# Kernel tuning notes

Measured on AMD Instinct MI355X. Metric: run time of the kernel, lower is better.

## Reference

```python
import jax, jax.numpy as jnp
import numpy as np
from itertools import combinations

B, T, D = 2, 2048, 1024
H, PD = 16, 4
DH = D // H
PAIRS = list(combinations(range(PD), 2))  # 6 pairs -> plucker_dim 6

_J6 = jnp.array([[0, 0, 0, 0, 0, 1], [0, 0, 0, 0, -1, 0], [0, 0, 0, 1, 0, 0],
                 [0, 0, 1, 0, 0, 0], [0, -1, 0, 0, 0, 0], [1, 0, 0, 0, 0, 0]],
                dtype=jnp.float32)


def exterior(p1, p2):
    # p1, p2: [B,T,H,PD] -> normalized Plucker coords [B,T,H,6]
    parts = [p1[..., i] * p2[..., j] - p1[..., j] * p2[..., i] for i, j in PAIRS]
    L = jnp.stack(parts, axis=-1)
    n = jnp.maximum(jnp.linalg.norm(L, axis=-1, keepdims=True), 1e-12)
    return L / n


def setup_inputs() -> dict:
    key = jax.random.key(0)
    ks = jax.random.split(key, 16)
    s = 0.02
    inp = {
        'x': jax.random.normal(ks[0], (B, T, D), jnp.float32),
        'qkv_w': jax.random.normal(ks[1], (D, 3 * D), jnp.float32) * s,
        'qkv_b': jnp.zeros((3 * D,), jnp.float32),
        'w1_write': jax.random.normal(ks[2], (D, PD * H), jnp.float32) * s,
        'w2_write': jax.random.normal(ks[3], (D, PD * H), jnp.float32) * s,
        'w1_read': jax.random.normal(ks[4], (D, PD * H), jnp.float32) * s,
        'w2_read': jax.random.normal(ks[5], (D, PD * H), jnp.float32) * s,
        'memv_w': jax.random.normal(ks[6], (D, D), jnp.float32) * s,
        'memv_b': jnp.zeros((D,), jnp.float32),
        'memg_w': jax.random.normal(ks[7], (D, H), jnp.float32) * s,
        'memg_b': jnp.zeros((H,), jnp.float32),
        'mem_scale': jnp.full((H,), 0.1, jnp.float32),
        'out_w': jax.random.normal(ks[8], (D, D), jnp.float32) * s,
        'out_b': jnp.zeros((D,), jnp.float32),
        'J': _J6,
        'decays': jnp.array([0.95] * (H // 2) + [0.999] * (H - H // 2), jnp.float32),
    }
    return inp


def reference(x, qkv_w, qkv_b, w1_write, w2_write, w1_read, w2_read,
              memv_w, memv_b, memg_w, memg_b, mem_scale, out_w, out_b, J, decays):
    Bx, Tx, Dx = x.shape
    scale = DH ** -0.5

    # --- standard causal attention branch ---
    qkv = (x @ qkv_w + qkv_b).reshape(Bx, Tx, 3, H, DH)
    q, k, v = qkv[:, :, 0], qkv[:, :, 1], qkv[:, :, 2]  # [B,T,H,dh]
    scores = jnp.einsum('bihd,bjhd->bhij', q, k) * scale
    i = jnp.arange(Tx)
    causal = i[:, None] >= i[None, :]  # keep j <= i
    scores = jnp.where(causal[None, None], scores, -jnp.inf)
    attn = jax.nn.softmax(scores, axis=-1)
    seq_out = jnp.einsum('bhij,bjhd->bihd', attn, v).reshape(Bx, Tx, Dx)

    # --- Plucker memory branch ---
    x_prev = jnp.concatenate([jnp.zeros((Bx, 1, Dx), x.dtype), x[:, :-1]], axis=1)
    w1 = (x_prev @ w1_write).reshape(Bx, Tx, H, PD)
    w2 = (x @ w2_write).reshape(Bx, Tx, H, PD)
    write_lines = exterior(w1, w2)          # [B,T,H,6]
    r1 = (x @ w1_read).reshape(Bx, Tx, H, PD)
    r2 = (x @ w2_read).reshape(Bx, Tx, H, PD)
    read_lines = exterior(r1, r2)           # [B,T,H,6]

    Jw = jnp.einsum('bthi,ij->bthj', write_lines, J)
    incidence = jnp.einsum('bihp,bjhp->bhij', read_lines, Jw)  # [B,H,T,T]
    inc_sq = incidence ** 2

    diffs = i[:, None] - i[None, :]                      # [T,T]
    lower = diffs > 0                                    # strictly past (j < i)
    dsafe = jnp.where(lower, diffs, 0).astype(x.dtype)
    weights = jnp.where(lower[None], decays[:, None, None] ** dsafe[None], 0.0)  # [H,T,T]
    mem_score = jnp.sum(inc_sq * weights[None], axis=-1)  # [B,H,T]

    mem_val = x @ memv_w + memv_b                         # [B,T,D]
    gate = jax.nn.sigmoid(x @ memg_w + memg_b)            # [B,T,H]
    gated = jax.nn.sigmoid(mem_score.transpose(0, 2, 1) * mem_scale[None, None]) * gate
    gated = jnp.mean(gated, axis=-1, keepdims=True)       # [B,T,1]

    return (seq_out + gated * mem_val) @ out_w + out_b
```

## Files before the change

### kernel.cpp

```cpp
#include <hip/hip_runtime.h>

#define BT 4096
#define Dd 1024
#define Tt 2048

typedef __attribute__((ext_vector_type(8))) short bf16x8;
typedef __attribute__((ext_vector_type(4))) float f32x4;
typedef __attribute__((ext_vector_type(4))) unsigned u32x4;

__device__ __forceinline__ short f2bf(float f) {
  unsigned u = __builtin_bit_cast(unsigned, f);
  u = (u + 0x7FFFu + ((u >> 16) & 1u)) >> 16;
  return (short)u;
}
__device__ __forceinline__ float bf2f(short s) {
  unsigned u = ((unsigned)(unsigned short)s) << 16;
  return __builtin_bit_cast(float, u);
}
__device__ __forceinline__ unsigned cvt_pk_bf16(float a, float b) {
  unsigned r;
  asm("v_cvt_pk_bf16_f32 %0, %1, %2" : "=v"(r) : "v"(a), "v"(b));
  return r;
}

__device__ __forceinline__ void load_lds16(const void* gsrc, void* ldst) {
  __builtin_amdgcn_global_load_lds(
      (const __attribute__((address_space(1))) void*)gsrc,
      (__attribute__((address_space(3))) void*)ldst, 16, 0, 0);
}

__global__ __launch_bounds__(256) void k_wtall(
    const float* __restrict__ qkv_w, const float* __restrict__ memv_w,
    const float* __restrict__ out_w, const float* __restrict__ w1w,
    const float* __restrict__ w2w, const float* __restrict__ w1r,
    const float* __restrict__ w2r, const float* __restrict__ memg_w,
    short* __restrict__ WTall, short* __restrict__ WTout,
    const float* __restrict__ x, short* __restrict__ xb) {
  __shared__ float tile[64][65];
  const int bid = blockIdx.x;
  if (bid >= 1360) {
    int i = (bid - 1360) * 256 + threadIdx.x;
    float4 v = ((const float4*)x)[i];
    short4 o;
    o.x = f2bf(v.x); o.y = f2bf(v.y); o.z = f2bf(v.z); o.w = f2bf(v.w);
    ((short4*)xb)[i] = o;
    return;
  }
  const float* src;
  short* dst;
  int N, n0, k0, rowoff;
  if (bid < 768) {
    src = qkv_w; dst = WTall; N = 3072;
    n0 = (bid % 48) * 64; k0 = (bid / 48) * 64; rowoff = 0;
  } else if (bid < 1024) {
    int r = bid - 768;
    src = memv_w; dst = WTall; N = 1024;
    n0 = (r % 16) * 64; k0 = (r / 16) * 64; rowoff = 3072;
  } else if (bid < 1280) {
    int r = bid - 1024;
    src = out_w; dst = WTout; N = 1024;
    n0 = (r % 16) * 64; k0 = (r / 16) * 64; rowoff = 0;
  } else {
    int r = bid - 1280;
    int z = r / 16;
    src = z == 0 ? w1w : z == 1 ? w2w : z == 2 ? w1r : z == 3 ? w2r : memg_w;
    dst = WTall; N = (z == 4) ? 16 : 64;
    n0 = 0; k0 = (r % 16) * 64; rowoff = 4096 + z * 64;
  }
  const int c = threadIdx.x & 63, r4 = threadIdx.x >> 6;
#pragma unroll
  for (int i = 0; i < 16; ++i) {
    int r = i * 4 + r4;
    float v = 0.f;
    if (n0 + c < N) v = src[(size_t)(k0 + r) * N + n0 + c];
    tile[r][c] = v;
  }
  __syncthreads();
#pragma unroll
  for (int i = 0; i < 16; ++i) {
    int n = i * 4 + r4;
    if (n0 + n < N)
      dst[(size_t)(rowoff + n0 + n) * 1024 + k0 + c] = f2bf(tile[c][n]);
  }
}

__global__ __launch_bounds__(256, 4) void k_g128(
    const short* __restrict__ A, const short* __restrict__ Bt,
    const float* __restrict__ bias, const float* __restrict__ bias2,
    short* __restrict__ oq, short* __restrict__ ok_, short* __restrict__ ov,
    short* __restrict__ omv, float* __restrict__ ocs, int K) {
  __shared__ __align__(16) short lds[16384];
  const int tid = threadIdx.x;
  const int wid = tid >> 6, lane = tid & 63;
  const int wr = wid >> 1, wc = wid & 1;
  const int ql = lane & 15, g = lane >> 4;
  int wg = blockIdx.x, xcd = wg & 7, idx = wg >> 3;
  const int n_t = idx >> 2;
  const int m_t = xcd * 4 + (idx & 3);
  const int nkt = K >> 5;
  const int bm = m_t * 128, bn = n_t * 128;
  f32x4 acc[4][4] = {};

  const short* srcA[2];
  const short* srcB[2];
  short* dstA[2];
  short* dstB[2];
#pragma unroll
  for (int j = 0; j < 2; ++j) {
    int o16 = j * 256 + tid;
    int rr = o16 >> 2, u = o16 & 3;
    int sp = u ^ ((rr >> 1) & 3);
    srcA[j] = A + (size_t)(bm + rr) * K + sp * 8;
    srcB[j] = Bt + (size_t)(bn + rr) * K + sp * 8;
    dstA[j] = lds + o16 * 8;
    dstB[j] = lds + 8192 + o16 * 8;
  }
#define STG(D, KT)                                                            \
  do {                                                                        \
    const int k0s = (KT) << 5;                                                \
    _Pragma("unroll") for (int j = 0; j < 2; ++j) {                           \
      load_lds16(srcA[j] + k0s, dstA[j] + (D)*4096);                          \
      load_lds16(srcB[j] + k0s, dstB[j] + (D)*4096);                          \
    }                                                                         \
  } while (0)

  const int sw = (g ^ ((ql >> 1) & 3)) << 4;
  const char* bA = (const char*)lds + wr * 4096 + ql * 64 + sw;
  const char* bB = (const char*)lds + 16384 + wc * 4096 + ql * 64 + sw;

#define RD_A(DST, DOFF, MQ)                                                    \
  _Pragma("unroll") for (int mi = 0; mi < 2; ++mi)                             \
      DST[mi] = *(const bf16x8*)(bA + (DOFF) + (MQ)*2048 + mi * 1024);
#define RD_B(DST, DOFF, NQ)                                                    \
  _Pragma("unroll") for (int ni = 0; ni < 2; ++ni)                             \
      DST[ni] = *(const bf16x8*)(bB + (DOFF) + (NQ)*2048 + ni * 1024);
#define MFMA4(AF, BF, MQ, NQ)                                                  \
  _Pragma("unroll") for (int mi = 0; mi < 2; ++mi)                             \
      _Pragma("unroll") for (int ni = 0; ni < 2; ++ni)                         \
          acc[(MQ)*2 + mi][(NQ)*2 + ni] =                                      \
      __builtin_amdgcn_mfma_f32_16x16x32_bf16(                                 \
          BF[ni], AF[mi], acc[(MQ)*2 + mi][(NQ)*2 + ni], 0, 0, 0)

  STG(0, 0);

  for (int kt = 0; kt < nkt; ++kt) {
    const int d = kt & 1;
    const int dOff = d << 13;
    const bool s1 = kt + 1 < nkt;
    if (s1) {
      STG(d ^ 1, kt + 1);
      asm volatile("s_waitcnt vmcnt(4)" ::: "memory");
    } else {
      asm volatile("s_waitcnt vmcnt(0)" ::: "memory");
    }
    __builtin_amdgcn_sched_barrier(0);
    __builtin_amdgcn_s_barrier();
    bf16x8 a0[2], a1[2], b0[2], b1[2];
    RD_A(a0, dOff, 0);
    RD_A(a1, dOff, 1);
    RD_B(b0, dOff, 0);
    RD_B(b1, dOff, 1);
    asm volatile("s_waitcnt lgkmcnt(0)" ::: "memory");
    __builtin_amdgcn_sched_barrier(0);
    __builtin_amdgcn_s_setprio(1);
    MFMA4(a0, b0, 0, 0);
    MFMA4(a0, b1, 0, 1);
    MFMA4(a1, b1, 1, 1);
    MFMA4(a1, b0, 1, 0);
    __builtin_amdgcn_s_setprio(0);
    __builtin_amdgcn_sched_barrier(0);
    __builtin_amdgcn_s_barrier();
    __builtin_amdgcn_sched_barrier(0);
  }
#undef MFMA4
#undef RD_A
#undef RD_B
#undef STG

#pragma unroll
  for (int a = 0; a < 4; ++a) {
    const int m = bm + wr * 64 + a * 16 + ql;
    const int b = m >> 11, t = m & 2047;
#pragma unroll
    for (int c = 0; c < 4; ++c) {
      const int n0 = bn + wc * 64 + c * 16 + g * 4;
      f32x4 v = acc[a][c];
      if (n0 < 3072) {
        const float4 b4 = *(const float4*)&bias[n0];
        v[0] += b4.x; v[1] += b4.y; v[2] += b4.z; v[3] += b4.w;
        uint2 pk = make_uint2(cvt_pk_bf16(v[0], v[1]), cvt_pk_bf16(v[2], v[3]));
        const int sel = n0 >> 10, rem = n0 & 1023;
        if (sel == 0)
          *(uint2*)&oq[((size_t)(b * 16 + (rem >> 6)) * 2048 + t) * 64 + (rem & 63)] = pk;
        else if (sel == 1)
          *(uint2*)&ok_[((size_t)(b * 16 + (rem >> 6)) * 2048 + t) * 64 + (rem & 63)] = pk;
        else
          *(uint2*)&ov[(size_t)(b * 2048 + t) * 1024 + rem] = pk;
      } else if (n0 < 4096) {
        const float4 b4 = *(const float4*)&bias2[n0 - 3072];
        v[0] += b4.x; v[1] += b4.y; v[2] += b4.z; v[3] += b4.w;
        uint2 pk = make_uint2(cvt_pk_bf16(v[0], v[1]), cvt_pk_bf16(v[2], v[3]));
        *(uint2*)&omv[(size_t)(b * 2048 + t) * 1024 + n0 - 3072] = pk;
      } else if (n0 < 4368) {
        *(f32x4*)&ocs[(size_t)(b * 2048 + t) * 272 + n0 - 4096] = v;
      }
    }
  }
}

__global__ __launch_bounds__(256, 4) void k_gout(
    const short* __restrict__ A, const short* __restrict__ Bt,
    const float* __restrict__ bias, float* __restrict__ C, int K) {
  __shared__ __align__(16) short lds[8192];
  const int tid = threadIdx.x;
  const int wid = tid >> 6, lane = tid & 63;
  const int wr = wid >> 1, wc = wid & 1;
  const int ql = lane & 15, g = lane >> 4;
  int wg = blockIdx.x, xcd = wg & 7, idx = wg >> 3;
  const int n_t = idx >> 3, m_t = xcd * 8 + (idx & 7);
  const int bm = m_t * 64, bn = n_t * 64;
  const int nkt = K >> 5;
  f32x4 acc[2][2] = {};

  const short* srcA;
  const short* srcB;
  short* dstA;
  short* dstB;
  {
    int rr = tid >> 2, u = tid & 3;
    int sp = u ^ ((rr >> 1) & 3);
    srcA = A + (size_t)(bm + rr) * K + sp * 8;
    srcB = Bt + (size_t)(bn + rr) * K + sp * 8;
    dstA = lds + tid * 8;
    dstB = lds + 4096 + tid * 8;
  }
#define STG(D, KT)                                                            \
  do {                                                                        \
    const int k0s = (KT) << 5;                                                \
    load_lds16(srcA + k0s, dstA + (D)*2048);                                  \
    load_lds16(srcB + k0s, dstB + (D)*2048);                                  \
  } while (0)

  const int sw = (g ^ ((ql >> 1) & 3)) << 4;
  const char* bA = (const char*)lds + wr * 2048 + ql * 64 + sw;
  const char* bB = (const char*)lds + 8192 + wc * 2048 + ql * 64 + sw;

  STG(0, 0);

  for (int kt = 0; kt < nkt; ++kt) {
    const int d = kt & 1;
    const int dOff = d << 12;
    const bool s1 = kt + 1 < nkt;
    if (s1) {
      STG(d ^ 1, kt + 1);
      asm volatile("s_waitcnt vmcnt(2)" ::: "memory");
    } else {
      asm volatile("s_waitcnt vmcnt(0)" ::: "memory");
    }
    __builtin_amdgcn_sched_barrier(0);
    __builtin_amdgcn_s_barrier();
    bf16x8 af[2], bf2[2];
#pragma unroll
    for (int mi = 0; mi < 2; ++mi)
      af[mi] = *(const bf16x8*)(bA + dOff + mi * 1024);
#pragma unroll
    for (int ni = 0; ni < 2; ++ni)
      bf2[ni] = *(const bf16x8*)(bB + dOff + ni * 1024);
    asm volatile("s_waitcnt lgkmcnt(0)" ::: "memory");
    __builtin_amdgcn_sched_barrier(0);
    __builtin_amdgcn_s_setprio(1);
#pragma unroll
    for (int mi = 0; mi < 2; ++mi)
#pragma unroll
      for (int ni = 0; ni < 2; ++ni)
        acc[mi][ni] = __builtin_amdgcn_mfma_f32_16x16x32_bf16(
            bf2[ni], af[mi], acc[mi][ni], 0, 0, 0);
    __builtin_amdgcn_s_setprio(0);
    __builtin_amdgcn_sched_barrier(0);
    __builtin_amdgcn_s_barrier();
    __builtin_amdgcn_sched_barrier(0);
  }
#undef STG

#pragma unroll
  for (int a = 0; a < 2; ++a) {
    const int m = bm + wr * 32 + a * 16 + ql;
#pragma unroll
    for (int c = 0; c < 2; ++c) {
      const int n0 = bn + wc * 32 + c * 16 + g * 4;
      f32x4 v = acc[a][c];
      const float4 b4 = *(const float4*)&bias[n0];
      v[0] += b4.x; v[1] += b4.y; v[2] += b4.z; v[3] += b4.w;
      *(f32x4*)&C[(size_t)m * 1024 + n0] = v;
    }
  }
}

__global__ __launch_bounds__(256) void k_vtrans(const short* __restrict__ vtmp,
                                                short* __restrict__ vb) {
  __shared__ short tile[64][68];
  const int bh = blockIdx.x, b = bh >> 4, h = bh & 15;
  const int t0 = blockIdx.y * 64;
  const int tid = threadIdx.x;
#pragma unroll
  for (int pass = 0; pass < 16; ++pass) {
    int r = pass * 4 + (tid >> 6);
    int c = tid & 63;
    tile[r][c] = vtmp[((size_t)(b * 2048) + t0 + r) * 1024 + h * 64 + c];
  }
  __syncthreads();
#pragma unroll
  for (int pass = 0; pass < 16; ++pass) {
    int r = pass * 4 + (tid >> 6);
    int c = tid & 63;
    int cp = (c & 32) | (((c >> 2) & 3) << 3) | (((c >> 4) & 1) << 2) | (c & 3);
    vb[(((size_t)b * 16 + h) * 64 + r) * 2048 + t0 + cp] = tile[c][r];
  }
}

#define ATT_SCALE 0.18033688f

__device__ __forceinline__ void attn_core(const bf16x8 qa[2], f32x4 o[4],
                                          float& m, float& l,
                                          const short* __restrict__ Kc,
                                          const short* __restrict__ Vc,
                                          int qt, int kt, int qglob,
                                          int ql, int g) {
  const int kv0 = kt * 64;
  f32x4 s4[4];
  __builtin_amdgcn_s_setprio(1);
#pragma unroll
  for (int nt = 0; nt < 4; ++nt) {
    int krow = nt * 16 + ql;
    f32x4 s = {0.f, 0.f, 0.f, 0.f};
#pragma unroll
    for (int kc = 0; kc < 2; ++kc) {
      int sl = (kc * 4 + g) ^ (krow & 7);
      bf16x8 af = *(const bf16x8*)&Kc[krow * 64 + sl * 8];
      s = __builtin_amdgcn_mfma_f32_16x16x32_bf16(af, qa[kc], s, 0, 0, 0);
    }
    s4[nt] = s;
  }
  __builtin_amdgcn_s_setprio(0);
  float mt = -1e30f;
  const bool diag = (kt == qt);
#pragma unroll
  for (int nt = 0; nt < 4; ++nt)
#pragma unroll
    for (int rg = 0; rg < 4; ++rg) {
      float v = s4[nt][rg] * ATT_SCALE;
      if (diag) {
        int kk = kv0 + nt * 16 + g * 4 + rg;
        v = (kk <= qglob) ? v : -1e30f;
      }
      s4[nt][rg] = v;
      mt = fmaxf(mt, v);
    }
  mt = fmaxf(mt, __shfl_xor(mt, 16, 64));
  mt = fmaxf(mt, __shfl_xor(mt, 32, 64));
  float mnew = fmaxf(m, mt);
  float sf = __builtin_amdgcn_exp2f(m - mnew);
  m = mnew;
  float rs = 0.f;
#pragma unroll
  for (int nt = 0; nt < 4; ++nt)
#pragma unroll
    for (int rg = 0; rg < 4; ++rg) {
      float p = __builtin_amdgcn_exp2f(s4[nt][rg] - mnew);
      s4[nt][rg] = p;
      rs += p;
    }
  rs += __shfl_xor(rs, 16, 64);
  rs += __shfl_xor(rs, 32, 64);
  l = l * sf + rs;
#pragma unroll
  for (int nt = 0; nt < 4; ++nt) o[nt] *= sf;
  bf16x8 pf[2];
#pragma unroll
  for (int kc = 0; kc < 2; ++kc) {
    u32x4 w;
    w[0] = cvt_pk_bf16(s4[2 * kc][0], s4[2 * kc][1]);
    w[1] = cvt_pk_bf16(s4[2 * kc][2], s4[2 * kc][3]);
    w[2] = cvt_pk_bf16(s4[2 * kc + 1][0], s4[2 * kc + 1][1]);
    w[3] = cvt_pk_bf16(s4[2 * kc + 1][2], s4[2 * kc + 1][3]);
    pf[kc] = __builtin_bit_cast(bf16x8, w);
  }
  __builtin_amdgcn_s_setprio(1);
#pragma unroll
  for (int nt2 = 0; nt2 < 4; ++nt2) {
    int d = nt2 * 16 + ql;
#pragma unroll
    for (int kc = 0; kc < 2; ++kc) {
      int sl = (kc * 4 + g) ^ (d & 7);
      bf16x8 vf = *(const bf16x8*)&Vc[d * 64 + sl * 8];
      o[nt2] = __builtin_amdgcn_mfma_f32_16x16x32_bf16(vf, pf[kc], o[nt2], 0, 0, 0);
    }
  }
  __builtin_amdgcn_s_setprio(0);
}

__device__ __forceinline__ void attn_epi(const f32x4 o[4], float l,
                                         short* __restrict__ Fb,
                                         const short* __restrict__ mvb,
                                         const float* __restrict__ gm,
                                         float* ep,
                                         int b, int h, int qt, int wave, int lane) {
  const int ql = lane & 15, g = lane >> 4;
  float inv = 1.f / l;
#pragma unroll
  for (int nt2 = 0; nt2 < 4; ++nt2) {
    f32x4 v = o[nt2] * inv;
    *(f32x4*)&ep[ql * 64 + (((nt2 * 4 + g) ^ (ql & 7)) << 2)] = v;
  }
  const size_t rowbase = ((size_t)b * 2048 + qt * 64 + wave * 16);
  short* srow = Fb + rowbase * 1024 + h * 64;
  const short* mrow = mvb + rowbase * 1024 + h * 64;
  const float* grow = gm + rowbase;
#pragma unroll
  for (int p = 0; p < 8; ++p) {
    int prow = p * 2 + (lane >> 5);
    int d2 = (lane & 31) * 2;
    const float* rp = &ep[prow * 64 + (((d2 >> 2) ^ (prow & 7)) << 2) + (d2 & 3)];
    float2 vv = *(const float2*)rp;
    float gg = grow[prow];
    unsigned mvp = *(const unsigned*)&mrow[(size_t)prow * 1024 + d2];
    float m0 = bf2f((short)(mvp & 0xffff));
    float m1 = bf2f((short)(mvp >> 16));
    *(unsigned*)&srow[(size_t)prow * 1024 + d2] =
        cvt_pk_bf16(vv.x + gg * m0, vv.y + gg * m1);
  }
}

__global__ __launch_bounds__(256, 4) void k_attn(const short* __restrict__ Q,
                                                 const short* __restrict__ Kg,
                                                 const short* __restrict__ Vg,
                                                 const short* __restrict__ mvb,
                                                 const float* __restrict__ gm,
                                                 short* __restrict__ Fb) {
  __shared__ short Kt[2][64 * 64];
  __shared__ short Vt[2][64 * 64];
  const int wg = blockIdx.x;
  const int x = wg & 7, r = wg >> 3;
  const int q = r >> 2, j = r & 3;
  const int bh = 4 * x + j;
  const int q2 = (q + 16) & 31;
  const int qt = (j == 0) ? q : (j == 1) ? 31 - q : (j == 2) ? q2 : 31 - q2;
  const int b = bh >> 4, h = bh & 15;
  const int tid = threadIdx.x;
  const int wave = tid >> 6, lane = tid & 63;
  const int ql = lane & 15, g = lane >> 4;
  const int qglob = qt * 64 + wave * 16 + ql;
  const short* qr = Q + ((size_t)bh * 2048 + qglob) * 64;
  bf16x8 qa[2];
  qa[0] = *(const bf16x8*)&qr[g * 8];
  qa[1] = *(const bf16x8*)&qr[32 + g * 8];
  f32x4 o[4] = {};
  float m = -1e30f, l = 0.f;
  const short* kgb = Kg + (size_t)bh * 2048 * 64;
  const short* vgb = Vg + (size_t)bh * 64 * 2048;

  auto stage = [&](int buf, int kt) {
    int kv0 = kt * 64;
#pragma unroll
    for (int jj = 0; jj < 2; ++jj) {
      int slot = (wave * 2 + jj) * 64 + lane;
      int rr = slot >> 3, s8 = slot & 7;
      int ss = s8 ^ (rr & 7);
      load_lds16(kgb + (size_t)(kv0 + rr) * 64 + ss * 8, &Kt[buf][slot * 8]);
      load_lds16(vgb + (size_t)rr * 2048 + kv0 + ss * 8, &Vt[buf][slot * 8]);
    }
  };

  stage(0, 0);
  int cur = 0;
  for (int it = 0; it <= qt; ++it) {
    __syncthreads();
    if (it < qt) stage(cur ^ 1, it + 1);
    attn_core(qa, o, m, l, Kt[cur], Vt[cur], qt, it, qglob, ql, g);
    cur ^= 1;
  }
  __syncthreads();
  float* ep = (float*)&Kt[0][0] + wave * 1024;
  attn_epi(o, l, Fb, mvb, gm, ep, b, h, qt, wave, lane);
}

__global__ __launch_bounds__(256) void k_lines(const float* __restrict__ Cs,
                                               const float* __restrict__ Jm,
                                               float* __restrict__ u,
                                               float* __restrict__ rr) {
  int idx = blockIdx.x * 256 + threadIdx.x;
  if (idx >= 2 * 2048 * 16) return;
  int h = idx & 15, t = (idx >> 4) & 2047, b = idx >> 15;
  const float* rowx = Cs + (size_t)(b * 2048 + t) * 272;
  float w1[4], w2[4], r1[4], r2[4];
  if (t == 0) {
#pragma unroll
    for (int i = 0; i < 4; ++i) w1[i] = 0.f;
  } else {
    const float* prev = Cs + (size_t)(b * 2048 + t - 1) * 272;
#pragma unroll
    for (int i = 0; i < 4; ++i) w1[i] = prev[h * 4 + i];
  }
#pragma unroll
  for (int i = 0; i < 4; ++i) {
    w2[i] = rowx[64 + h * 4 + i];
    r1[i] = rowx[128 + h * 4 + i];
    r2[i] = rowx[192 + h * 4 + i];
  }
  const int pi[6] = {0, 0, 0, 1, 1, 2}, pj[6] = {1, 2, 3, 2, 3, 3};
  float wl[6], rl[6], nw = 0.f, nr = 0.f;
#pragma unroll
  for (int e = 0; e < 6; ++e) {
    wl[e] = w1[pi[e]] * w2[pj[e]] - w1[pj[e]] * w2[pi[e]];
    rl[e] = r1[pi[e]] * r2[pj[e]] - r1[pj[e]] * r2[pi[e]];
    nw += wl[e] * wl[e];
    nr += rl[e] * rl[e];
  }
  nw = 1.f / fmaxf(sqrtf(nw), 1e-12f);
  nr = 1.f / fmaxf(sqrtf(nr), 1e-12f);
  size_t base = (((size_t)b * 16 + h) * 2048 + t) * 6;
#pragma unroll
  for (int jc = 0; jc < 6; ++jc) {
    float s = 0.f;
#pragma unroll
    for (int i = 0; i < 6; ++i) s += wl[i] * Jm[i * 6 + jc];
    u[base + jc] = s * nw;
    rr[base + jc] = rl[jc] * nr;
  }
}

__global__ __launch_bounds__(256) void k_scanw(const float* __restrict__ u,
                                               float* __restrict__ w,
                                               const float* __restrict__ decays) {
  __shared__ float wtot[4];
  const int ch = blockIdx.x;
  const int bh = blockIdx.y;
  const float d = decays[bh & 15];
  const int p = ch / 6, q = ch % 6;
  const int tid = threadIdx.x, lane = tid & 63, wv = tid >> 6;
  const float* ub = u + (size_t)bh * 2048 * 6;
  const int t0 = tid * 8;
  float z[8];
  float a = 0.f;
#pragma unroll
  for (int i = 0; i < 8; ++i) {
    float up = ub[(t0 + i) * 6 + p], uq = ub[(t0 + i) * 6 + q];
    z[i] = up * uq;
    a = d * (a + z[i]);
  }
  float d8 = d * d; d8 *= d8; d8 *= d8;
  float I = a;
  float ds = d8;
#pragma unroll
  for (int s = 1; s < 64; s <<= 1) {
    float v = __shfl_up(I, s, 64);
    if (lane >= s) I += ds * v;
    ds *= ds;
  }
  if (lane == 63) wtot[wv] = I;
  __syncthreads();
  float carry = 0.f;
  for (int w2 = 0; w2 < wv; ++w2) carry = carry * ds + wtot[w2];
  float dlp1 = exp2f(log2f(d8) * (float)(lane + 1));
  float Ig = I + dlp1 * carry;
  float E = __shfl_up(Ig, 1, 64);
  if (lane == 0) E = carry;
  float S = E;
  float out[8];
#pragma unroll
  for (int i = 0; i < 8; ++i) {
    out[i] = S;
    S = d * (S + z[i]);
  }
  float4* wp = (float4*)(w + ((size_t)bh * 36 + ch) * 2048 + t0);
  wp[0] = make_float4(out[0], out[1], out[2], out[3]);
  wp[1] = make_float4(out[4], out[5], out[6], out[7]);
}

__global__ __launch_bounds__(256) void k_scandot(const float* __restrict__ rr,
                                                 const float* __restrict__ w,
                                                 float* __restrict__ scores) {
  const int bh = blockIdx.y;
  const int t = blockIdx.x * 256 + threadIdx.x;
  const float* rb = rr + ((size_t)bh * 2048 + t) * 6;
  float r[6];
#pragma unroll
  for (int i = 0; i < 6; ++i) r[i] = rb[i];
  const float* wb = w + (size_t)bh * 36 * 2048 + t;
  float acc = 0.f;
#pragma unroll
  for (int ch = 0; ch < 36; ++ch)
    acc += r[ch / 6] * r[ch % 6] * wb[(size_t)ch * 2048];
  scores[(size_t)bh * 2048 + t] = acc;
}

__global__ __launch_bounds__(256) void k_gate(const float* __restrict__ scores,
                                              const float* __restrict__ Cs,
                                              const float* __restrict__ memg_b,
                                              const float* __restrict__ mem_scale,
                                              float* __restrict__ gmean) {
  int idx = blockIdx.x * 256 + threadIdx.x;
  if (idx >= BT) return;
  int b = idx >> 11, t = idx & 2047;
  float acc = 0.f;
#pragma unroll
  for (int h = 0; h < 16; ++h) {
    float s = scores[((size_t)(b * 16 + h) * 2048) + t];
    float gl = Cs[(size_t)idx * 272 + 256 + h] + memg_b[h];
    float a = 1.f / (1.f + __expf(-s * mem_scale[h]));
    float gg = 1.f / (1.f + __expf(-gl));
    acc += a * gg;
  }
  gmean[idx] = acc * (1.f / 16.f);
}

extern "C" void kernel_launch(void* const* d_in, const int* in_sizes, int n_in,
                              void* d_out, int out_size, void* d_ws, size_t ws_size,
                              hipStream_t stream) {
  const float* x = (const float*)d_in[0];
  const float* qkv_w = (const float*)d_in[1];
  const float* qkv_b = (const float*)d_in[2];
  const float* w1w = (const float*)d_in[3];
  const float* w2w = (const float*)d_in[4];
  const float* w1r = (const float*)d_in[5];
  const float* w2r = (const float*)d_in[6];
  const float* memv_w = (const float*)d_in[7];
  const float* memv_b = (const float*)d_in[8];
  const float* memg_w = (const float*)d_in[9];
  const float* memg_b = (const float*)d_in[10];
  const float* mem_scale = (const float*)d_in[11];
  const float* out_w = (const float*)d_in[12];
  const float* out_b = (const float*)d_in[13];
  const float* Jm = (const float*)d_in[14];
  const float* decays = (const float*)d_in[15];

  char* w = (char*)d_ws;
  size_t off = 0;
  auto alloc = [&](size_t bytes) -> void* {
    void* p = w + off;
    off += (bytes + 255) & ~(size_t)255;
    return p;
  };
  short* xb = (short*)alloc((size_t)BT * Dd * 2);
  short* WTall = (short*)alloc((size_t)4480 * 1024 * 2);
  short* WTout = (short*)alloc((size_t)1024 * 1024 * 2);
  short* qb = (short*)alloc((size_t)32 * 2048 * 64 * 2);
  short* kb = (short*)alloc((size_t)32 * 2048 * 64 * 2);
  short* vtmp = (short*)alloc((size_t)BT * 1024 * 2);
  short* vb = (short*)alloc((size_t)32 * 64 * 2048 * 2);
  float* Csm = (float*)alloc((size_t)BT * 272 * 4);
  float* ua = (float*)alloc((size_t)32 * 2048 * 6 * 4);
  float* ra = (float*)alloc((size_t)32 * 2048 * 6 * 4);
  float* sc = (float*)alloc((size_t)32 * 2048 * 4);
  float* gm = (float*)alloc((size_t)BT * 4);
  short* mvb = (short*)alloc((size_t)BT * 1024 * 2);
  short* Fb = (short*)alloc((size_t)BT * Dd * 2);
  float* wscan = (float*)alloc((size_t)32 * 36 * 2048 * 4);
  (void)ws_size; (void)in_sizes; (void)n_in; (void)out_size;

  k_wtall<<<5456, 256, 0, stream>>>(qkv_w, memv_w, out_w, w1w, w2w, w1r, w2r,
                                    memg_w, WTall, WTout, x, xb);

  k_g128<<<1120, 256, 0, stream>>>(xb, WTall, qkv_b, memv_b,
                                   qb, kb, vtmp, mvb, Csm, 1024);

  k_lines<<<(2 * 2048 * 16 + 255) / 256, 256, 0, stream>>>(Csm, Jm, ua, ra);
  k_scanw<<<dim3(36, 32), 256, 0, stream>>>(ua, wscan, decays);
  k_scandot<<<dim3(8, 32), 256, 0, stream>>>(ra, wscan, sc);
  k_gate<<<(BT + 255) / 256, 256, 0, stream>>>(sc, Csm, memg_b, mem_scale, gm);

  k_vtrans<<<dim3(32, 32), 256, 0, stream>>>(vtmp, vb);

  k_attn<<<1024, 256, 0, stream>>>(qb, kb, vb, mvb, gm, Fb);

  k_gout<<<1024, 256, 0, stream>>>(Fb, WTout, out_b, (float*)d_out, 1024);
}
```

Measured before the change: 155.4 us.

## Fuse small kernels, prescale Q in GEMM epilogue, skip redundant softmax rescale

Merges the Plücker-line kernel and the V transpose into one launch, and merges the scan-dot and gate kernels into one, removing two launches and the scores buffer. The attention scale now multiplies Q in the QKV GEMM epilogue, so the per-score multiply in attention goes away. The online softmax skips the exp and the rescale of the accumulator when no row max increases, at the cost of a wave-wide vote and a branch. The fused scan-gate kernel runs only 32 blocks with a serial loop over heads, which may leave most of the GPU idle for that stage.

```diff
diff --git a/kernel.cpp b/kernel.cpp
--- a/kernel.cpp
+++ b/kernel.cpp
@@ -3,6 +3,7 @@
 #define BT 4096
 #define Dd 1024
 #define Tt 2048
+#define ATT_SCALE 0.18033688f
 
 typedef __attribute__((ext_vector_type(8))) short bf16x8;
 typedef __attribute__((ext_vector_type(4))) float f32x4;
@@ -188,14 +189,18 @@
       if (n0 < 3072) {
         const float4 b4 = *(const float4*)&bias[n0];
         v[0] += b4.x; v[1] += b4.y; v[2] += b4.z; v[3] += b4.w;
-        uint2 pk = make_uint2(cvt_pk_bf16(v[0], v[1]), cvt_pk_bf16(v[2], v[3]));
         const int sel = n0 >> 10, rem = n0 & 1023;
-        if (sel == 0)
+        if (sel == 0) {
+          v[0] *= ATT_SCALE; v[1] *= ATT_SCALE; v[2] *= ATT_SCALE; v[3] *= ATT_SCALE;
+          uint2 pk = make_uint2(cvt_pk_bf16(v[0], v[1]), cvt_pk_bf16(v[2], v[3]));
           *(uint2*)&oq[((size_t)(b * 16 + (rem >> 6)) * 2048 + t) * 64 + (rem & 63)] = pk;
-        else if (sel == 1)
+        } else if (sel == 1) {
+          uint2 pk = make_uint2(cvt_pk_bf16(v[0], v[1]), cvt_pk_bf16(v[2], v[3]));
           *(uint2*)&ok_[((size_t)(b * 16 + (rem >> 6)) * 2048 + t) * 64 + (rem & 63)] = pk;
-        else
+        } else {
+          uint2 pk = make_uint2(cvt_pk_bf16(v[0], v[1]), cvt_pk_bf16(v[2], v[3]));
           *(uint2*)&ov[(size_t)(b * 2048 + t) * 1024 + rem] = pk;
+        }
       } else if (n0 < 4096) {
         const float4 b4 = *(const float4*)&bias2[n0 - 3072];
         v[0] += b4.x; v[1] += b4.y; v[2] += b4.z; v[3] += b4.w;
@@ -296,29 +301,74 @@
   }
 }
 
-__global__ __launch_bounds__(256) void k_vtrans(const short* __restrict__ vtmp,
-                                                short* __restrict__ vb) {
+__global__ __launch_bounds__(256) void k_lv(const float* __restrict__ Cs,
+                                            const float* __restrict__ Jm,
+                                            float* __restrict__ u,
+                                            float* __restrict__ rr,
+                                            const short* __restrict__ vtmp,
+                                            short* __restrict__ vb) {
   __shared__ short tile[64][68];
-  const int bh = blockIdx.x, b = bh >> 4, h = bh & 15;
-  const int t0 = blockIdx.y * 64;
-  const int tid = threadIdx.x;
-#pragma unroll
-  for (int pass = 0; pass < 16; ++pass) {
-    int r = pass * 4 + (tid >> 6);
-    int c = tid & 63;
-    tile[r][c] = vtmp[((size_t)(b * 2048) + t0 + r) * 1024 + h * 64 + c];
-  }
-  __syncthreads();
-#pragma unroll
-  for (int pass = 0; pass < 16; ++pass) {
-    int r = pass * 4 + (tid >> 6);
-    int c = tid & 63;
-    int cp = (c & 32) | (((c >> 2) & 3) << 3) | (((c >> 4) & 1) << 2) | (c & 3);
-    vb[(((size_t)b * 16 + h) * 64 + r) * 2048 + t0 + cp] = tile[c][r];
-  }
-}
-
-#define ATT_SCALE 0.18033688f
+  const int bid = blockIdx.x;
+  if (bid >= 256) {
+    const int r2 = bid - 256;
+    const int bh = r2 >> 5, b = bh >> 4, h = bh & 15;
+    const int t0 = (r2 & 31) * 64;
+    const int tid = threadIdx.x;
+#pragma unroll
+    for (int pass = 0; pass < 16; ++pass) {
+      int r = pass * 4 + (tid >> 6);
+      int c = tid & 63;
+      tile[r][c] = vtmp[((size_t)(b * 2048) + t0 + r) * 1024 + h * 64 + c];
+    }
+    __syncthreads();
+#pragma unroll
+    for (int pass = 0; pass < 16; ++pass) {
+      int r = pass * 4 + (tid >> 6);
+      int c = tid & 63;
+      int cp = (c & 32) | (((c >> 2) & 3) << 3) | (((c >> 4) & 1) << 2) | (c & 3);
+      vb[(((size_t)b * 16 + h) * 64 + r) * 2048 + t0 + cp] = tile[c][r];
+    }
+    return;
+  }
+  int idx = bid * 256 + threadIdx.x;
+  int h = idx & 15, t = (idx >> 4) & 2047, b = idx >> 15;
+  const float* rowx = Cs + (size_t)(b * 2048 + t) * 272;
+  float w1[4], w2[4], r1[4], r2v[4];
+  if (t == 0) {
+#pragma unroll
+    for (int i = 0; i < 4; ++i) w1[i] = 0.f;
+  } else {
+    const float* prev = Cs + (size_t)(b * 2048 + t - 1) * 272;
+#pragma unroll
+    for (int i = 0; i < 4; ++i) w1[i] = prev[h * 4 + i];
+  }
+#pragma unroll
+  for (int i = 0; i < 4; ++i) {
+    w2[i] = rowx[64 + h * 4 + i];
+    r1[i] = rowx[128 + h * 4 + i];
+    r2v[i] = rowx[192 + h * 4 + i];
+  }
+  const int pi[6] = {0, 0, 0, 1, 1, 2}, pj[6] = {1, 2, 3, 2, 3, 3};
+  float wl[6], rl[6], nw = 0.f, nr = 0.f;
+#pragma unroll
+  for (int e = 0; e < 6; ++e) {
+    wl[e] = w1[pi[e]] * w2[pj[e]] - w1[pj[e]] * w2[pi[e]];
+    rl[e] = r1[pi[e]] * r2v[pj[e]] - r1[pj[e]] * r2v[pi[e]];
+    nw += wl[e] * wl[e];
+    nr += rl[e] * rl[e];
+  }
+  nw = 1.f / fmaxf(sqrtf(nw), 1e-12f);
+  nr = 1.f / fmaxf(sqrtf(nr), 1e-12f);
+  size_t base = (((size_t)b * 16 + h) * 2048 + t) * 6;
+#pragma unroll
+  for (int jc = 0; jc < 6; ++jc) {
+    float s = 0.f;
+#pragma unroll
+    for (int i = 0; i < 6; ++i) s += wl[i] * Jm[i * 6 + jc];
+    u[base + jc] = s * nw;
+    rr[base + jc] = rl[jc] * nr;
+  }
+}
 
 __device__ __forceinline__ void attn_core(const bf16x8 qa[2], f32x4 o[4],
                                           float& m, float& l,
@@ -348,7 +398,7 @@
   for (int nt = 0; nt < 4; ++nt)
 #pragma unroll
     for (int rg = 0; rg < 4; ++rg) {
-      float v = s4[nt][rg] * ATT_SCALE;
+      float v = s4[nt][rg];
       if (diag) {
         int kk = kv0 + nt * 16 + g * 4 + rg;
         v = (kk <= qglob) ? v : -1e30f;
@@ -359,22 +409,25 @@
   mt = fmaxf(mt, __shfl_xor(mt, 16, 64));
   mt = fmaxf(mt, __shfl_xor(mt, 32, 64));
   float mnew = fmaxf(m, mt);
-  float sf = __builtin_amdgcn_exp2f(m - mnew);
-  m = mnew;
+  if (__any(mnew > m)) {
+    float sf = __builtin_amdgcn_exp2f(m - mnew);
+    m = mnew;
+    l *= sf;
+#pragma unroll
+    for (int nt = 0; nt < 4; ++nt) o[nt] *= sf;
+  }
   float rs = 0.f;
 #pragma unroll
   for (int nt = 0; nt < 4; ++nt)
 #pragma unroll
     for (int rg = 0; rg < 4; ++rg) {
-      float p = __builtin_amdgcn_exp2f(s4[nt][rg] - mnew);
+      float p = __builtin_amdgcn_exp2f(s4[nt][rg] - m);
       s4[nt][rg] = p;
       rs += p;
     }
   rs += __shfl_xor(rs, 16, 64);
   rs += __shfl_xor(rs, 32, 64);
-  l = l * sf + rs;
-#pragma unroll
-  for (int nt = 0; nt < 4; ++nt) o[nt] *= sf;
+  l += rs;
   bf16x8 pf[2];
 #pragma unroll
   for (int kc = 0; kc < 2; ++kc) {
@@ -484,51 +537,6 @@
   attn_epi(o, l, Fb, mvb, gm, ep, b, h, qt, wave, lane);
 }
 
-__global__ __launch_bounds__(256) void k_lines(const float* __restrict__ Cs,
-                                               const float* __restrict__ Jm,
-                                               float* __restrict__ u,
-                                               float* __restrict__ rr) {
-  int idx = blockIdx.x * 256 + threadIdx.x;
-  if (idx >= 2 * 2048 * 16) return;
-  int h = idx & 15, t = (idx >> 4) & 2047, b = idx >> 15;
-  const float* rowx = Cs + (size_t)(b * 2048 + t) * 272;
-  float w1[4], w2[4], r1[4], r2[4];
-  if (t == 0) {
-#pragma unroll
-    for (int i = 0; i < 4; ++i) w1[i] = 0.f;
-  } else {
-    const float* prev = Cs + (size_t)(b * 2048 + t - 1) * 272;
-#pragma unroll
-    for (int i = 0; i < 4; ++i) w1[i] = prev[h * 4 + i];
-  }
-#pragma unroll
-  for (int i = 0; i < 4; ++i) {
-    w2[i] = rowx[64 + h * 4 + i];
-    r1[i] = rowx[128 + h * 4 + i];
-    r2[i] = rowx[192 + h * 4 + i];
-  }
-  const int pi[6] = {0, 0, 0, 1, 1, 2}, pj[6] = {1, 2, 3, 2, 3, 3};
-  float wl[6], rl[6], nw = 0.f, nr = 0.f;
-#pragma unroll
-  for (int e = 0; e < 6; ++e) {
-    wl[e] = w1[pi[e]] * w2[pj[e]] - w1[pj[e]] * w2[pi[e]];
-    rl[e] = r1[pi[e]] * r2[pj[e]] - r1[pj[e]] * r2[pi[e]];
-    nw += wl[e] * wl[e];
-    nr += rl[e] * rl[e];
-  }
-  nw = 1.f / fmaxf(sqrtf(nw), 1e-12f);
-  nr = 1.f / fmaxf(sqrtf(nr), 1e-12f);
-  size_t base = (((size_t)b * 16 + h) * 2048 + t) * 6;
-#pragma unroll
-  for (int jc = 0; jc < 6; ++jc) {
-    float s = 0.f;
-#pragma unroll
-    for (int i = 0; i < 6; ++i) s += wl[i] * Jm[i * 6 + jc];
-    u[base + jc] = s * nw;
-    rr[base + jc] = rl[jc] * nr;
-  }
-}
-
 __global__ __launch_bounds__(256) void k_scanw(const float* __restrict__ u,
                                                float* __restrict__ w,
                                                const float* __restrict__ decays) {
@@ -577,35 +585,27 @@
   wp[1] = make_float4(out[4], out[5], out[6], out[7]);
 }
 
-__global__ __launch_bounds__(256) void k_scandot(const float* __restrict__ rr,
-                                                 const float* __restrict__ w,
-                                                 float* __restrict__ scores) {
-  const int bh = blockIdx.y;
-  const int t = blockIdx.x * 256 + threadIdx.x;
-  const float* rb = rr + ((size_t)bh * 2048 + t) * 6;
-  float r[6];
-#pragma unroll
-  for (int i = 0; i < 6; ++i) r[i] = rb[i];
-  const float* wb = w + (size_t)bh * 36 * 2048 + t;
-  float acc = 0.f;
-#pragma unroll
-  for (int ch = 0; ch < 36; ++ch)
-    acc += r[ch / 6] * r[ch % 6] * wb[(size_t)ch * 2048];
-  scores[(size_t)bh * 2048 + t] = acc;
-}
-
-__global__ __launch_bounds__(256) void k_gate(const float* __restrict__ scores,
-                                              const float* __restrict__ Cs,
-                                              const float* __restrict__ memg_b,
-                                              const float* __restrict__ mem_scale,
-                                              float* __restrict__ gmean) {
-  int idx = blockIdx.x * 256 + threadIdx.x;
-  if (idx >= BT) return;
+__global__ __launch_bounds__(128) void k_sg(const float* __restrict__ rr,
+                                            const float* __restrict__ w,
+                                            const float* __restrict__ Cs,
+                                            const float* __restrict__ memg_b,
+                                            const float* __restrict__ mem_scale,
+                                            float* __restrict__ gmean) {
+  int idx = blockIdx.x * 128 + threadIdx.x;
   int b = idx >> 11, t = idx & 2047;
   float acc = 0.f;
-#pragma unroll
+#pragma unroll 1
   for (int h = 0; h < 16; ++h) {
-    float s = scores[((size_t)(b * 16 + h) * 2048) + t];
+    const int bh = b * 16 + h;
+    const float* rb = rr + ((size_t)bh * 2048 + t) * 6;
+    float r[6];
+#pragma unroll
+    for (int i = 0; i < 6; ++i) r[i] = rb[i];
+    const float* wb = w + (size_t)bh * 36 * 2048 + t;
+    float s = 0.f;
+#pragma unroll
+    for (int ch = 0; ch < 36; ++ch)
+      s += r[ch / 6] * r[ch % 6] * wb[(size_t)ch * 2048];
     float gl = Cs[(size_t)idx * 272 + 256 + h] + memg_b[h];
     float a = 1.f / (1.f + __expf(-s * mem_scale[h]));
     float gg = 1.f / (1.f + __expf(-gl));
@@ -651,7 +651,6 @@
   float* Csm = (float*)alloc((size_t)BT * 272 * 4);
   float* ua = (float*)alloc((size_t)32 * 2048 * 6 * 4);
   float* ra = (float*)alloc((size_t)32 * 2048 * 6 * 4);
-  float* sc = (float*)alloc((size_t)32 * 2048 * 4);
   float* gm = (float*)alloc((size_t)BT * 4);
   short* mvb = (short*)alloc((size_t)BT * 1024 * 2);
   short* Fb = (short*)alloc((size_t)BT * Dd * 2);
@@ -664,12 +663,10 @@
   k_g128<<<1120, 256, 0, stream>>>(xb, WTall, qkv_b, memv_b,
                                    qb, kb, vtmp, mvb, Csm, 1024);
 
-  k_lines<<<(2 * 2048 * 16 + 255) / 256, 256, 0, stream>>>(Csm, Jm, ua, ra);
+  k_lv<<<1280, 256, 0, stream>>>(Csm, Jm, ua, ra, vtmp, vb);
+
   k_scanw<<<dim3(36, 32), 256, 0, stream>>>(ua, wscan, decays);
-  k_scandot<<<dim3(8, 32), 256, 0, stream>>>(ra, wscan, sc);
-  k_gate<<<(BT + 255) / 256, 256, 0, stream>>>(sc, Csm, memg_b, mem_scale, gm);
-
-  k_vtrans<<<dim3(32, 32), 256, 0, stream>>>(vtmp, vb);
+  k_sg<<<32, 128, 0, stream>>>(ra, wscan, Csm, memg_b, mem_scale, gm);
 
   k_attn<<<1024, 256, 0, stream>>>(qb, kb, vb, mvb, gm, Fb);
 
```

After: 162.5 us. 4.6% more time.
